# Performance work log

Measured on AMD Instinct MI355X. Metric: run time of the kernel, lower is better.

## Reference

```python
import jax, jax.numpy as jnp
import numpy as np

NUM_NODES = 3072
NUM_RELATIONS = 8
NUM_GRAPHS = 16


def setup_inputs() -> dict:
    key = jax.random.key(0)
    k1, k2, k3, k4 = jax.random.split(key, 4)
    z = jax.random.normal(k1, (NUM_NODES, NUM_RELATIONS), dtype=jnp.float32)
    seg_matrix = jax.random.randint(k2, (NUM_NODES, NUM_NODES), 0, 2, dtype=jnp.int32)
    cls_label = jax.random.randint(k3, (NUM_NODES,), 0, 27, dtype=jnp.int64)
    batch = jnp.sort(jax.random.randint(k4, (NUM_NODES,), 0, NUM_GRAPHS, dtype=jnp.int64))
    return {"z": z, "seg_matrix": seg_matrix, "cls_label": cls_label, "batch": batch}


def reference(z, seg_matrix, cls_label, batch):
    # z: [N, R]; seg_matrix: [N, N]; cls_label, batch: [N]
    N, R = z.shape
    # seg_matrix += eye(N); seg_mask = (seg_matrix == 0)
    seg = seg_matrix.astype(z.dtype) + jnp.eye(N, dtype=z.dtype)
    seg_mask = seg == 0
    # node_mask: exclude class labels 24, 25, 26
    node_mask = (cls_label != 24) & (cls_label != 25) & (cls_label != 26)
    # pairs must lie in the same graph of the batch (the per-i loop in torch)
    same_batch = batch[:, None] == batch[None, :]
    pair_mask = node_mask[:, None] & node_mask[None, :] & same_batch & seg_mask  # [N, N]
    # default result: one-hot on relation 0
    default = jnp.concatenate(
        [jnp.ones((1,), dtype=z.dtype), jnp.zeros((R - 1,), dtype=z.dtype)]
    )  # [R], broadcasts over [N, N, R]
    # selected pairs get elementwise product z[row] * z[col]
    outer = z[:, None, :] * z[None, :, :]  # [N, N, R]
    return jnp.where(pair_mask[:, :, None], outer, default)
```

## Files before the change

### kernel.cpp

```cpp
#include <hip/hip_runtime.h>
#include <hip/hip_bf16.h>

#define NN 3072
#define RR 8

typedef float f4 __attribute__((ext_vector_type(4)));

__global__ __launch_bounds__(256) void fill_default(f4* __restrict__ out)
{
    const int t = blockIdx.x * 256 + threadIdx.x;
    f4 v;
    v.x = (t & 1) ? 0.0f : 1.0f;
    v.y = 0.0f; v.z = 0.0f; v.w = 0.0f;
    out[t] = v;
}

__global__ __launch_bounds__(256) void scatter_pairs(
    const float* __restrict__ z,
    const int*   __restrict__ seg,
    const int*   __restrict__ cls,
    const int*   __restrict__ batch,
    float*       __restrict__ out)
{
    const int i    = (blockIdx.x * 256 + threadIdx.x) >> 6;
    const int lane = threadIdx.x & 63;

    const int ci = cls[i];
    if (ci >= 24) return;
    const int bi = batch[i];

    int l = 0, r = NN;
    while (l < r) { const int m = (l + r) >> 1; if (batch[m] <  bi) l = m + 1; else r = m; }
    const int lo = l;
    r = NN;
    while (l < r) { const int m = (l + r) >> 1; if (batch[m] <= bi) l = m + 1; else r = m; }
    const int hi = l;

    const f4* zip = (const f4*)(z + (long long)i * RR);
    const f4 a0 = zip[0], a1 = zip[1];
    const long long rowbase = (long long)i * NN;

    for (int j = lo + lane; j < hi; j += 64) {
        const int s = seg[rowbase + j];
        const bool pm = (s == 0) & (i != j) & (cls[j] < 24);
        if (pm) {
            const f4* zjp = (const f4*)(z + (long long)j * RR);
            f4* o = (f4*)(out + (rowbase + j) * RR);
            o[0] = a0 * zjp[0];
            o[1] = a1 * zjp[1];
        }
    }
}

extern "C" void kernel_launch(void* const* d_in, const int* in_sizes, int n_in,
                              void* d_out, int out_size, void* d_ws, size_t ws_size,
                              hipStream_t stream) {
    const float* z     = (const float*)d_in[0];
    const int*   seg   = (const int*)d_in[1];
    const int*   cls   = (const int*)d_in[2];
    const int*   batch = (const int*)d_in[3];
    float* out = (float*)d_out;

    fill_default<<<(NN * NN * 2) / 256, 256, 0, stream>>>((f4*)out);

    scatter_pairs<<<(NN * 64) / 256, 256, 0, stream>>>(z, seg, cls, batch, out);
}
```

Before: 60.68 us.

## Fuse default fill and pair scatter into one single-write kernel

Replaces the two-kernel approach (fill the whole output with the default, then overwrite selected pairs) with one kernel on a 2D grid. For each row, 24 blocks write defaults only outside the row's batch segment, and a 25th block writes every in-segment entry exactly once, either the product or the default. This avoids writing the in-segment region twice and drops a kernel launch. The trade-off is one block per row handling the whole in-segment span with 128 pairs per iteration, which may leave that work unevenly spread.

```diff
diff --git a/kernel.cpp b/kernel.cpp
--- a/kernel.cpp
+++ b/kernel.cpp
@@ -6,28 +6,30 @@
 
 typedef float f4 __attribute__((ext_vector_type(4)));
 
-__global__ __launch_bounds__(256) void fill_default(f4* __restrict__ out)
-{
-    const int t = blockIdx.x * 256 + threadIdx.x;
-    f4 v;
-    v.x = (t & 1) ? 0.0f : 1.0f;
-    v.y = 0.0f; v.z = 0.0f; v.w = 0.0f;
-    out[t] = v;
-}
-
-__global__ __launch_bounds__(256) void scatter_pairs(
+__global__ __launch_bounds__(256) void frd_onepass(
     const float* __restrict__ z,
     const int*   __restrict__ seg,
     const int*   __restrict__ cls,
     const int*   __restrict__ batch,
     float*       __restrict__ out)
 {
-    const int i    = (blockIdx.x * 256 + threadIdx.x) >> 6;
-    const int lane = threadIdx.x & 63;
+    const int i  = blockIdx.y;
+    const int bi = batch[i];
+    const long long rowout = (long long)i * (NN * RR);
+    const int h = threadIdx.x & 1;
 
-    const int ci = cls[i];
-    if (ci >= 24) return;
-    const int bi = batch[i];
+    if (blockIdx.x < 24) {
+        const int t = blockIdx.x * 256 + threadIdx.x;
+        const int j = t >> 1;
+        const int bj = batch[j];
+        if (bj != bi) {
+            f4 v;
+            v.x = h ? 0.0f : 1.0f;
+            v.y = 0.0f; v.z = 0.0f; v.w = 0.0f;
+            *(f4*)(out + rowout + (long long)t * 4) = v;
+        }
+        return;
+    }
 
     int l = 0, r = NN;
     while (l < r) { const int m = (l + r) >> 1; if (batch[m] <  bi) l = m + 1; else r = m; }
@@ -36,19 +38,25 @@
     while (l < r) { const int m = (l + r) >> 1; if (batch[m] <= bi) l = m + 1; else r = m; }
     const int hi = l;
 
-    const f4* zip = (const f4*)(z + (long long)i * RR);
-    const f4 a0 = zip[0], a1 = zip[1];
-    const long long rowbase = (long long)i * NN;
+    const bool rowok = (cls[i] < 24);
+    f4 a = {0.0f, 0.0f, 0.0f, 0.0f};
+    if (rowok) a = *(const f4*)(z + i * RR + h * 4);
 
-    for (int j = lo + lane; j < hi; j += 64) {
-        const int s = seg[rowbase + j];
-        const bool pm = (s == 0) & (i != j) & (cls[j] < 24);
-        if (pm) {
-            const f4* zjp = (const f4*)(z + (long long)j * RR);
-            f4* o = (f4*)(out + (rowbase + j) * RR);
-            o[0] = a0 * zjp[0];
-            o[1] = a1 * zjp[1];
+    f4 dflt;
+    dflt.x = h ? 0.0f : 1.0f;
+    dflt.y = 0.0f; dflt.z = 0.0f; dflt.w = 0.0f;
+
+    for (int p = lo + (threadIdx.x >> 1); p < hi; p += 128) {
+        f4 res = dflt;
+        if (rowok) {
+            const int s = seg[(long long)i * NN + p];
+            const bool pm = (s == 0) & (i != p) & (cls[p] < 24);
+            if (pm) {
+                const f4 b = *(const f4*)(z + p * RR + h * 4);
+                res = a * b;
+            }
         }
+        *(f4*)(out + rowout + (long long)p * 8 + h * 4) = res;
     }
 }
 
@@ -61,7 +69,6 @@
     const int*   batch = (const int*)d_in[3];
     float* out = (float*)d_out;
 
-    fill_default<<<(NN * NN * 2) / 256, 256, 0, stream>>>((f4*)out);
-
-    scatter_pairs<<<(NN * 64) / 256, 256, 0, stream>>>(z, seg, cls, batch, out);
+    dim3 grid(25, NN);
+    frd_onepass<<<grid, dim3(256), 0, stream>>>(z, seg, cls, batch, out);
 }
```

Result: faster. 58.30 us (-3.9%).
